# Kernel tuning notes

Measured on AMD Instinct MI355X. Metric: run time of the kernel, lower is better.

The kernel has to match this reference:

```python
import jax, jax.numpy as jnp
import numpy as np

VOCAB, H, B, L = 32000, 1024, 64, 256  # L leaves per complete binary tree


def setup_inputs() -> dict:
    key = jax.random.key(0)
    ks = jax.random.split(key, 12)
    s = 1.0 / np.sqrt(H)
    return {
        "tokens": jax.random.randint(ks[0], (B, L), 0, VOCAB),
        "emb":    jax.random.normal(ks[1], (VOCAB, H), jnp.float32) * 0.02,
        "W_iock": jax.random.normal(ks[2], (H, 3 * H), jnp.float32) * s,
        "b_iock": jax.random.normal(ks[3], (3 * H,), jnp.float32) * s,
        "U_iock": jax.random.normal(ks[4], (H, 3 * H), jnp.float32) * s,
        "W_fl":   jax.random.normal(ks[5], (H, H), jnp.float32) * s,
        "b_fl":   jax.random.normal(ks[6], (H,), jnp.float32) * s,
        "U_fl":   jax.random.normal(ks[7], (H, H), jnp.float32) * s,
        "W_fr":   jax.random.normal(ks[8], (H, H), jnp.float32) * s,
        "b_fr":   jax.random.normal(ks[9], (H,), jnp.float32) * s,
        "U_fr":   jax.random.normal(ks[10], (H, H), jnp.float32) * s,
    }


def _tree_lstm_levels(h, c, W_iock, b_iock, U_iock, W_fl, b_fl, U_fl, W_fr, b_fr, U_fr):
    """Bottom-up level sweep over a complete binary tree.

    h, c: (B, n, H) states of the current level. Each pass merges sibling
    pairs with the BinaryTreeLSTMCell.calculate gate math.
    """
    outs = []
    while h.shape[1] > 1:
        hl, hr = h[:, 0::2], h[:, 1::2]          # (B, n/2, H)
        cl, cr = c[:, 0::2], c[:, 1::2]
        # iock = W_iock(h_left) + U_iock(h_right); split -> i, o, c~
        iock = hl @ W_iock + hr @ U_iock + b_iock
        i_g, o_g, ck = jnp.split(iock, 3, axis=-1)
        fl = jax.nn.sigmoid(hl @ W_fl + hr @ U_fl + b_fl)
        fr = jax.nn.sigmoid(hl @ W_fr + hr @ U_fr + b_fr)
        c = jax.nn.sigmoid(i_g) * jnp.tanh(ck) + fl * cl + fr * cr
        h = jax.nn.sigmoid(o_g) * jnp.tanh(c)
        outs.append(h)
    forest_output = jnp.concatenate(outs, axis=1)  # (B, L-1, H) internal-node hiddens
    return forest_output, h, c


def reference(tokens, emb, W_iock, b_iock, U_iock, W_fl, b_fl, U_fl, W_fr, b_fr, U_fr):
    h = emb[tokens]                 # leaf hidden = embedding, (B, L, H)
    c = jnp.zeros_like(h)           # leaf memory cell = zeros
    forest_output, h_root, c_root = _tree_lstm_levels(
        h, c, W_iock, b_iock, U_iock, W_fl, b_fl, U_fl, W_fr, b_fr, U_fr)
    # (forest_output, (h, c)) with h, c as (1, B, H) like transpose(0, 1)
    return forest_output, (h_root.transpose(1, 0, 2), c_root.transpose(1, 0, 2))
```

## Files before the change

kernel.cpp:

```cpp
#include <hip/hip_runtime.h>
#include <stdint.h>

#define H     1024
#define K2    2048
#define NTOT  5120
#define BATCH 64
#define BM 128
#define BN 128
#define BK 64

typedef unsigned short u16;
typedef __attribute__((ext_vector_type(8))) short short8;
typedef __attribute__((ext_vector_type(4))) float floatx4;

__device__ __forceinline__ float bf2f(u16 u) {
    return __uint_as_float(((uint32_t)u) << 16);
}
__device__ __forceinline__ u16 f2bf(float f) {
    uint32_t u = __float_as_uint(f);
    u += 0x7fffu + ((u >> 16) & 1u);
    return (u16)(u >> 16);
}
__device__ __forceinline__ uint32_t pk2(float lo, float hi) {
    return (uint32_t)f2bf(lo) | ((uint32_t)f2bf(hi) << 16);
}
__device__ __forceinline__ float sigf(float x) {
    return 1.0f / (1.0f + __expf(-x));
}
__device__ __forceinline__ float tanh_(float x) {
    float e = __expf(-2.0f * fabsf(x));
    float r = (1.0f - e) / (1.0f + e);
    return copysignf(r, x);
}

__global__ void fuse_pre(const float* __restrict__ Wio, const float* __restrict__ Uio,
                         const float* __restrict__ Wfl, const float* __restrict__ Ufl,
                         const float* __restrict__ Wfr, const float* __restrict__ Ufr,
                         u16* __restrict__ WT,
                         const int* __restrict__ tokens, const float* __restrict__ emb,
                         u16* __restrict__ leaf) {
    __shared__ u16 tile[32][33];
    int blk = blockIdx.x;
    int t = threadIdx.x;
    if (blk < 10240) {
        int k0 = (blk & 63) * 32;
        int n0 = (blk >> 6) * 32;
        const float *Wp, *Up; int ncols, nloc;
        if (n0 < 3072)      { Wp = Wio; Up = Uio; ncols = 3072; nloc = n0; }
        else if (n0 < 4096) { Wp = Wfl; Up = Ufl; ncols = 1024; nloc = n0 - 3072; }
        else                { Wp = Wfr; Up = Ufr; ncols = 1024; nloc = n0 - 4096; }
        int c = t & 31, r = t >> 5;
#pragma unroll
        for (int i = 0; i < 4; ++i) {
            int rr = r + i * 8;
            int k = k0 + rr;
            float v = (k < 1024) ? Wp[(long)k * ncols + nloc + c]
                                 : Up[(long)(k - 1024) * ncols + nloc + c];
            tile[rr][c] = f2bf(v);
        }
        __syncthreads();
#pragma unroll
        for (int i = 0; i < 4; ++i) {
            int rr = r + i * 8;
            WT[(long)(n0 + rr) * K2 + k0 + c] = tile[c][rr];
        }
    } else {
        int idx = (blk - 10240) * 256 + t;
        int node = idx >> 8;
        int d4 = idx & 255;
        int tok = tokens[node];
        float4 v = ((const float4*)emb)[(long)tok * 256 + d4];
        uint2 o; o.x = pk2(v.x, v.y); o.y = pk2(v.z, v.w);
        ((uint2*)leaf)[(long)node * 256 + d4] = o;
    }
}

__global__ void gemm_bt(const u16* __restrict__ A, const u16* __restrict__ BT,
                        float* __restrict__ G, int mc) {
    __shared__ __align__(16) u16 AsBs[16896];
    u16* As = AsBs;
    u16* Bs = AsBs + 8192;
    float* epi = (float*)AsBs;
    int tid  = threadIdx.x;
    int lane = tid & 63;
    int w    = tid >> 6;
    int wm   = w >> 1, wn = w & 1;
    int rowTile = blockIdx.x * BM;
    int n0      = blockIdx.y * BN;

    const u16* asrc[4];
    const u16* bsrc[4];
#pragma unroll
    for (int cc = 0; cc < 4; ++cc) {
        int r = cc * 32 + w * 8 + (lane >> 3);
        int j = rowTile + r; if (j >= mc) j = mc - 1;
        asrc[cc] = A + (long)j * K2 + (lane & 7) * 8;
        bsrc[cc] = BT + (long)(n0 + r) * K2 + (lane & 7) * 8;
    }

    floatx4 acc[4][4];
#pragma unroll
    for (int mt = 0; mt < 4; ++mt)
#pragma unroll
        for (int nt = 0; nt < 4; ++nt)
            acc[mt][nt] = (floatx4){0.f, 0.f, 0.f, 0.f};

    for (int k0 = 0; k0 < K2; k0 += BK) {
#pragma unroll
        for (int cc = 0; cc < 4; ++cc) {
            __builtin_amdgcn_global_load_lds(
                (const __attribute__((address_space(1))) void*)(asrc[cc] + k0),
                (__attribute__((address_space(3))) void*)(As + cc * 2048 + w * 512), 16, 0, 0);
            __builtin_amdgcn_global_load_lds(
                (const __attribute__((address_space(1))) void*)(bsrc[cc] + k0),
                (__attribute__((address_space(3))) void*)(Bs + cc * 2048 + w * 512), 16, 0, 0);
        }
        __syncthreads();
#pragma unroll
        for (int kb = 0; kb < 2; ++kb) {
            int kfo = kb * 32 + (lane >> 4) * 8;
            short8 af[4], bfv[4];
#pragma unroll
            for (int mt = 0; mt < 4; ++mt)
                af[mt] = *(const short8*)&As[(wm * 64 + mt * 16 + (lane & 15)) * BK + kfo];
#pragma unroll
            for (int nt = 0; nt < 4; ++nt)
                bfv[nt] = *(const short8*)&Bs[(wn * 64 + nt * 16 + (lane & 15)) * BK + kfo];
#pragma unroll
            for (int mt = 0; mt < 4; ++mt)
#pragma unroll
                for (int nt = 0; nt < 4; ++nt)
                    acc[mt][nt] = __builtin_amdgcn_mfma_f32_16x16x32_bf16(
                        af[mt], bfv[nt], acc[mt][nt], 0, 0, 0);
        }
        __syncthreads();
    }

#pragma unroll
    for (int s = 0; s < 2; ++s) {
        if (wm == s) {
#pragma unroll
            for (int mt = 0; mt < 4; ++mt)
#pragma unroll
                for (int r = 0; r < 4; ++r) {
                    int lrow = mt * 16 + (lane >> 4) * 4 + r;
#pragma unroll
                    for (int nt = 0; nt < 4; ++nt)
                        epi[lrow * 132 + wn * 64 + nt * 16 + (lane & 15)] = acc[mt][nt][r];
                }
        }
        __syncthreads();
        int gr0 = rowTile + s * 64;
#pragma unroll
        for (int k = 0; k < 8; ++k) {
            int f4 = tid + k * 256;
            int row = f4 >> 5, c4 = f4 & 31;
            if (gr0 + row < mc) {
                float4 v = *(const float4*)&epi[row * 132 + c4 * 4];
                *(float4*)&G[(long)(gr0 + row) * NTOT + n0 + c4 * 4] = v;
            }
        }
        __syncthreads();
    }
}

#define SWZ2(r) (((r) >> 1) & 3)

#define GP_WAIT(VM)                                                                  \
    asm volatile("s_waitcnt vmcnt(" #VM ") lgkmcnt(0)\n\ts_barrier" ::: "memory")

__global__ __launch_bounds__(512, 4) void gemmP128(const u16* __restrict__ A,
                                                   const u16* __restrict__ BT,
                                                   const float* __restrict__ bio,
                                                   const float* __restrict__ bfl,
                                                   const float* __restrict__ bfr,
                                                   const void* __restrict__ c_in,
                                                   void* __restrict__ c_out, int c_bf16,
                                                   float* __restrict__ outF,
                                                   u16* __restrict__ hnext,
                                                   int lp, int level_off, int gm) {
    __shared__ __align__(16) u16 lds[28672];
    const int tid  = threadIdx.x;
    const int lane = tid & 63;
    const int w    = tid >> 6;
    const int wm   = w >> 1;
    const int wd   = w & 1;

    int f = blockIdx.x;
    int xcd = f & 7, c = f >> 3;
    int by = (xcd & 1) * 8 + (c & 7);
    int bx = (xcd >> 1) * (gm >> 2) + (c >> 3);
    long rowTile = (long)bx * 128;
    int d0 = by * 64;

    const u16* srcA[2];
    {
        int rr_ = w * 16 + (lane >> 2);
        int ck_ = ((lane & 3) ^ SWZ2(rr_)) * 8;
#pragma unroll
        for (int cc = 0; cc < 2; ++cc)
            srcA[cc] = A + (rowTile + rr_) * (long)K2 + cc * 32 + ck_;
    }
    const u16* srcB[5];
    {
        int sr_ = (w >> 1) * 16 + (lane >> 2);
        int ck_ = ((lane & 3) ^ SWZ2(sr_)) * 8;
#pragma unroll
        for (int g = 0; g < 5; ++g)
            srcB[g] = BT + (long)(g * 1024 + d0 + sr_) * K2 + (w & 1) * 32 + ck_;
    }

    const int qv = lane >> 4;
    int rA[2];
#pragma unroll
    for (int mf = 0; mf < 2; ++mf) {
        int rg = wm * 32 + mf * 16 + (lane & 15);
        rA[mf] = rg * 32 + ((qv ^ SWZ2(rg)) * 8);
    }
    int rB[2];
#pragma unroll
    for (int sub = 0; sub < 2; ++sub) {
        int rb = wd * 32 + sub * 16 + (lane & 15);
        rB[sub] = rb * 32 + ((qv ^ SWZ2(rb)) * 8);
    }

    floatx4 acc[2][10];
#pragma unroll
    for (int mf = 0; mf < 2; ++mf)
#pragma unroll
        for (int nf = 0; nf < 10; ++nf)
            acc[mf][nf] = (floatx4){0.f, 0.f, 0.f, 0.f};

#define GP_STG_A(TT)                                                                 \
    do {                                                                             \
        _Pragma("unroll")                                                            \
        for (int cc = 0; cc < 2; ++cc)                                               \
            __builtin_amdgcn_global_load_lds(                                        \
                (const __attribute__((address_space(1))) void*)(srcA[cc] + (TT) * 64),\
                (__attribute__((address_space(3))) void*)(lds + cc * 4096 + tid * 8), 16, 0, 0); \
    } while (0)

#define GP_STG_B(TT, GG)                                                             \
    __builtin_amdgcn_global_load_lds(                                                \
        (const __attribute__((address_space(1))) void*)(srcB[GG] + (TT) * 64),       \
        (__attribute__((address_space(3))) void*)(lds + 8192 + (GG) * 4096 + (w & 1) * 2048 + (w >> 1) * 512 + lane * 8), 16, 0, 0)

#define GP_MFMA(GG)                                                                  \
    do {                                                                             \
        __builtin_amdgcn_s_setprio(1);                                               \
        _Pragma("unroll")                                                            \
        for (int ks = 0; ks < 2; ++ks)                                               \
            _Pragma("unroll")                                                        \
            for (int mf = 0; mf < 2; ++mf)                                           \
                _Pragma("unroll")                                                    \
                for (int sub = 0; sub < 2; ++sub)                                    \
                    acc[mf][(GG) * 2 + sub] = __builtin_amdgcn_mfma_f32_16x16x32_bf16( \
                        aF[ks][mf], bF[ks][sub], acc[mf][(GG) * 2 + sub], 0, 0, 0);  \
        __builtin_amdgcn_s_setprio(0);                                               \
    } while (0)

#define GP_READ_A_B0()                                                               \
    do {                                                                             \
        _Pragma("unroll")                                                            \
        for (int ks = 0; ks < 2; ++ks) {                                             \
            _Pragma("unroll")                                                        \
            for (int mf = 0; mf < 2; ++mf)                                           \
                aF[ks][mf] = *(const short8*)&lds[rA[mf] + ks * 4096];               \
            _Pragma("unroll")                                                        \
            for (int sub = 0; sub < 2; ++sub)                                        \
                bF[ks][sub] = *(const short8*)&lds[8192 + ks * 2048 + rB[sub]];      \
        }                                                                            \
    } while (0)

#define GP_READ_B(GG)                                                                \
    do {                                                                             \
        _Pragma("unroll")                                                            \
        for (int ks = 0; ks < 2; ++ks)                                               \
            _Pragma("unroll")                                                        \
            for (int sub = 0; sub < 2; ++sub)                                        \
                bF[ks][sub] = *(const short8*)&lds[8192 + (GG) * 4096 + ks * 2048 + rB[sub]]; \
    } while (0)

    GP_STG_A(0);
    GP_STG_B(0, 0); GP_STG_B(0, 1); GP_STG_B(0, 2); GP_STG_B(0, 3);

    short8 aF[2][2], bF[2][2];
    for (int t = 0; t < 31; ++t) {
        GP_WAIT(3);
        GP_READ_A_B0();
        GP_STG_B(t, 4);
        GP_MFMA(0);
        GP_WAIT(3);
        GP_READ_B(1);
        GP_STG_A(t + 1);
        GP_MFMA(1);
        GP_WAIT(4);
        GP_READ_B(2);
        GP_STG_B(t + 1, 0);
        GP_MFMA(2);
        GP_WAIT(4);
        GP_READ_B(3);
        GP_STG_B(t + 1, 1);
        GP_MFMA(3);
        GP_WAIT(4);
        GP_READ_B(4);
        GP_STG_B(t + 1, 2);
        GP_STG_B(t + 1, 3);
        GP_MFMA(4);
    }
    GP_WAIT(3);
    GP_READ_A_B0();
    GP_STG_B(31, 4);
    GP_MFMA(0);
    GP_WAIT(3);
    GP_READ_B(1);
    GP_MFMA(1);
    GP_WAIT(2);
    GP_READ_B(2);
    GP_MFMA(2);
    GP_WAIT(1);
    GP_READ_B(3);
    GP_MFMA(3);
    GP_WAIT(0);
    GP_READ_B(4);
    GP_MFMA(4);

#undef GP_STG_A
#undef GP_STG_B
#undef GP_MFMA
#undef GP_READ_A_B0
#undef GP_READ_B

    float bI[2], bO[2], bC[2], bL[2], bR[2];
    int dsub[2];
#pragma unroll
    for (int sub = 0; sub < 2; ++sub) {
        int dd = d0 + wd * 32 + sub * 16 + (lane & 15);
        dsub[sub] = dd;
        bI[sub] = bio[dd]; bO[sub] = bio[1024 + dd]; bC[sub] = bio[2048 + dd];
        bL[sub] = bfl[dd]; bR[sub] = bfr[dd];
    }
    int pmask = (1 << lp) - 1;
    int has_c = (c_in != nullptr);
#pragma unroll
    for (int mf = 0; mf < 2; ++mf) {
#pragma unroll
        for (int rr = 0; rr < 4; ++rr) {
            int row = wm * 32 + mf * 16 + (lane >> 4) * 4 + rr;
            long J = rowTile + row;
            int b = (int)(J >> lp), p = (int)(J & pmask);
            long ho = ((long)b * 255 + level_off + p) * H;
#pragma unroll
            for (int sub = 0; sub < 2; ++sub) {
                int dd = dsub[sub];
                float i_  = acc[mf][0 + sub][rr] + bI[sub];
                float o_  = acc[mf][2 + sub][rr] + bO[sub];
                float ck_ = acc[mf][4 + sub][rr] + bC[sub];
                float cv = sigf(i_) * tanh_(ck_);
                if (has_c) {
                    float fl_ = sigf(acc[mf][6 + sub][rr] + bL[sub]);
                    float fr_ = sigf(acc[mf][8 + sub][rr] + bR[sub]);
                    float cl, cr;
                    if (c_bf16) {
                        cl = bf2f(__builtin_nontemporal_load(
                                 (const u16*)c_in + (2 * J) * H + dd));
                        cr = bf2f(__builtin_nontemporal_load(
                                 (const u16*)c_in + (2 * J + 1) * H + dd));
                    } else {
                        cl = __builtin_nontemporal_load(
                                 (const float*)c_in + (2 * J) * H + dd);
                        cr = __builtin_nontemporal_load(
                                 (const float*)c_in + (2 * J + 1) * H + dd);
                    }
                    cv += fl_ * cl + fr_ * cr;
                }
                float hv = sigf(o_) * tanh_(cv);
                __builtin_nontemporal_store(hv, &outF[ho + dd]);
                if (c_bf16)
                    __builtin_nontemporal_store(f2bf(cv), (u16*)c_out + J * H + dd);
                else
                    __builtin_nontemporal_store(cv, (float*)c_out + J * H + dd);
                __builtin_nontemporal_store(f2bf(hv), hnext + J * H + dd);
            }
        }
    }
}

__global__ __launch_bounds__(512, 4) void gemmS(const u16* __restrict__ A,
                                                const u16* __restrict__ BT,
                                                float* __restrict__ P,
                                                int RT, int KS, int NT,
                                                int mLim, int mPad) {
    __shared__ __align__(16) u16 lds[28672];
    const int tid  = threadIdx.x;
    const int lane = tid & 63;
    const int w    = tid >> 6;
    const int wm   = w >> 1;
    const int wd   = w & 1;

    int nwg = RT * 16 * KS;
    int f = blockIdx.x;
    int q = nwg >> 3, r = nwg & 7;
    int xcd = f & 7, rank = f >> 3;
    int wg = (xcd < r ? xcd * (q + 1) : r * (q + 1) + (xcd - r) * q) + rank;
    int bx  = wg % RT;
    int by  = (wg / RT) % 16;
    int ksx = wg / (RT * 16);
    long rowTile = (long)bx * 128;
    int d0 = by * 64;
    int kOff = ksx * (NT * 64);

    const u16* srcA[2];
    {
        int rr_ = w * 16 + (lane >> 2);
        int ck_ = ((lane & 3) ^ SWZ2(rr_)) * 8;
#pragma unroll
        for (int cc = 0; cc < 2; ++cc)
            srcA[cc] = A + (rowTile + rr_) * (long)K2 + kOff + cc * 32 + ck_;
    }
    const u16* srcB[5];
    {
        int sr_ = (w >> 1) * 16 + (lane >> 2);
        int ck_ = ((lane & 3) ^ SWZ2(sr_)) * 8;
#pragma unroll
        for (int g = 0; g < 5; ++g)
            srcB[g] = BT + (long)(g * 1024 + d0 + sr_) * K2 + kOff + (w & 1) * 32 + ck_;
    }

    const int qv = lane >> 4;
    int rA[2];
#pragma unroll
    for (int mf = 0; mf < 2; ++mf) {
        int rg = wm * 32 + mf * 16 + (lane & 15);
        rA[mf] = rg * 32 + ((qv ^ SWZ2(rg)) * 8);
    }
    int rB[2];
#pragma unroll
    for (int sub = 0; sub < 2; ++sub) {
        int rb = wd * 32 + sub * 16 + (lane & 15);
        rB[sub] = rb * 32 + ((qv ^ SWZ2(rb)) * 8);
    }

    floatx4 acc[2][10];
#pragma unroll
    for (int mf = 0; mf < 2; ++mf)
#pragma unroll
        for (int nf = 0; nf < 10; ++nf)
            acc[mf][nf] = (floatx4){0.f, 0.f, 0.f, 0.f};

#define GS_STG_A(TT)                                                                 \
    do {                                                                             \
        _Pragma("unroll")                                                            \
        for (int cc = 0; cc < 2; ++cc)                                               \
            __builtin_amdgcn_global_load_lds(                                        \
                (const __attribute__((address_space(1))) void*)(srcA[cc] + (TT) * 64),\
                (__attribute__((address_space(3))) void*)(lds + cc * 4096 + tid * 8), 16, 0, 0); \
    } while (0)

#define GS_STG_B(TT, GG)                                                             \
    __builtin_amdgcn_global_load_lds(                                                \
        (const __attribute__((address_space(1))) void*)(srcB[GG] + (TT) * 64),       \
        (__attribute__((address_space(3))) void*)(lds + 8192 + (GG) * 4096 + (w & 1) * 2048 + (w >> 1) * 512 + lane * 8), 16, 0, 0)

#define GS_MFMA(GG)                                                                  \
    do {                                                                             \
        __builtin_amdgcn_s_setprio(1);                                               \
        _Pragma("unroll")                                                            \
        for (int ks = 0; ks < 2; ++ks)                                               \
            _Pragma("unroll")                                                        \
            for (int mf = 0; mf < 2; ++mf)                                           \
                _Pragma("unroll")                                                    \
                for (int sub = 0; sub < 2; ++sub)                                    \
                    acc[mf][(GG) * 2 + sub] = __builtin_amdgcn_mfma_f32_16x16x32_bf16( \
                        aF[ks][mf], bF[ks][sub], acc[mf][(GG) * 2 + sub], 0, 0, 0);  \
        __builtin_amdgcn_s_setprio(0);                                               \
    } while (0)

#define GS_READ_A_B0()                                                               \
    do {                                                                             \
        _Pragma("unroll")                                                            \
        for (int ks = 0; ks < 2; ++ks) {                                             \
            _Pragma("unroll")                                                        \
            for (int mf = 0; mf < 2; ++mf)                                           \
                aF[ks][mf] = *(const short8*)&lds[rA[mf] + ks * 4096];               \
            _Pragma("unroll")                                                        \
            for (int sub = 0; sub < 2; ++sub)                                        \
                bF[ks][sub] = *(const short8*)&lds[8192 + ks * 2048 + rB[sub]];      \
        }                                                                            \
    } while (0)

#define GS_READ_B(GG)                                                                \
    do {                                                                             \
        _Pragma("unroll")                                                            \
        for (int ks = 0; ks < 2; ++ks)                                               \
            _Pragma("unroll")                                                        \
            for (int sub = 0; sub < 2; ++sub)                                        \
                bF[ks][sub] = *(const short8*)&lds[8192 + (GG) * 4096 + ks * 2048 + rB[sub]]; \
    } while (0)

    GS_STG_A(0);
    GS_STG_B(0, 0); GS_STG_B(0, 1); GS_STG_B(0, 2); GS_STG_B(0, 3);

    short8 aF[2][2], bF[2][2];
    for (int t = 0; t < NT - 1; ++t) {
        GP_WAIT(3);
        GS_READ_A_B0();
        GS_STG_B(t, 4);
        GS_MFMA(0);
        GP_WAIT(3);
        GS_READ_B(1);
        GS_STG_A(t + 1);
        GS_MFMA(1);
        GP_WAIT(4);
        GS_READ_B(2);
        GS_STG_B(t + 1, 0);
        GS_MFMA(2);
        GP_WAIT(4);
        GS_READ_B(3);
        GS_STG_B(t + 1, 1);
        GS_MFMA(3);
        GP_WAIT(4);
        GS_READ_B(4);
        GS_STG_B(t + 1, 2);
        GS_STG_B(t + 1, 3);
        GS_MFMA(4);
    }
    GP_WAIT(3);
    GS_READ_A_B0();
    GS_STG_B(NT - 1, 4);
    GS_MFMA(0);
    GP_WAIT(3);
    GS_READ_B(1);
    GS_MFMA(1);
    GP_WAIT(2);
    GS_READ_B(2);
    GS_MFMA(2);
    GP_WAIT(1);
    GS_READ_B(3);
    GS_MFMA(3);
    GP_WAIT(0);
    GS_READ_B(4);
    GS_MFMA(4);

#undef GS_STG_A
#undef GS_STG_B
#undef GS_MFMA
#undef GS_READ_A_B0
#undef GS_READ_B

    int dsub[2];
#pragma unroll
    for (int sub = 0; sub < 2; ++sub)
        dsub[sub] = d0 + wd * 32 + sub * 16 + (lane & 15);
#pragma unroll
    for (int mf = 0; mf < 2; ++mf) {
#pragma unroll
        for (int rr = 0; rr < 4; ++rr) {
            int row = wm * 32 + mf * 16 + (lane >> 4) * 4 + rr;
            long J = rowTile + row;
            if (J < mLim) {
                long pb = ((long)ksx * mPad + J) * NTOT;
#pragma unroll
                for (int g = 0; g < 5; ++g)
#pragma unroll
                    for (int sub = 0; sub < 2; ++sub)
                        P[pb + g * 1024 + dsub[sub]] = acc[mf][g * 2 + sub][rr];
            }
        }
    }
}

__global__ void redgate(const float* __restrict__ P, const float* __restrict__ bio,
                        const float* __restrict__ bfl, const float* __restrict__ bfr,
                        const void* __restrict__ c_in, void* __restrict__ c_out, int c_bf16,
                        float* __restrict__ outF, u16* __restrict__ hnext,
                        int lp, int level_off, int mc, int KS, int mPad) {
    int idx = blockIdx.x * 256 + threadIdx.x;
    int j = idx >> 8;
    if (j >= mc) return;
    int d = (idx & 255) * 4;
    int b = j >> lp, p = j & ((1 << lp) - 1);
    float ac[5][4] = {};
    for (int s = 0; s < KS; ++s) {
        long pb = ((long)s * mPad + j) * NTOT + d;
#pragma unroll
        for (int g = 0; g < 5; ++g) {
            float4 v = *(const float4*)&P[pb + g * 1024];
            ac[g][0] += v.x; ac[g][1] += v.y; ac[g][2] += v.z; ac[g][3] += v.w;
        }
    }
    float4 bi = *(const float4*)&bio[d];
    float4 bo = *(const float4*)&bio[1024 + d];
    float4 bc = *(const float4*)&bio[2048 + d];
    float4 bl = *(const float4*)&bfl[d];
    float4 br = *(const float4*)&bfr[d];
    const float* fbi = (const float*)&bi; const float* fbo = (const float*)&bo;
    const float* fbc = (const float*)&bc; const float* fbl = (const float*)&bl;
    const float* fbr = (const float*)&br;
    float clv[4], crv[4];
    {
        long cb = ((long)b * (2 << lp) + 2 * p) * H + d;
        if (c_bf16) {
            uint2 ul = *(const uint2*)((const u16*)c_in + cb);
            uint2 ur = *(const uint2*)((const u16*)c_in + cb + H);
            clv[0] = bf2f((u16)ul.x); clv[1] = bf2f((u16)(ul.x >> 16));
            clv[2] = bf2f((u16)ul.y); clv[3] = bf2f((u16)(ul.y >> 16));
            crv[0] = bf2f((u16)ur.x); crv[1] = bf2f((u16)(ur.x >> 16));
            crv[2] = bf2f((u16)ur.y); crv[3] = bf2f((u16)(ur.y >> 16));
        } else {
            float4 l4 = *(const float4*)((const float*)c_in + cb);
            float4 r4 = *(const float4*)((const float*)c_in + cb + H);
            clv[0] = l4.x; clv[1] = l4.y; clv[2] = l4.z; clv[3] = l4.w;
            crv[0] = r4.x; crv[1] = r4.y; crv[2] = r4.z; crv[3] = r4.w;
        }
    }
    float cv[4], hv[4];
#pragma unroll
    for (int qq = 0; qq < 4; ++qq) {
        float c = sigf(ac[0][qq] + fbi[qq]) * tanh_(ac[2][qq] + fbc[qq]);
        c += sigf(ac[3][qq] + fbl[qq]) * clv[qq] + sigf(ac[4][qq] + fbr[qq]) * crv[qq];
        cv[qq] = c;
        hv[qq] = sigf(ac[1][qq] + fbo[qq]) * tanh_(c);
    }
    long co = (long)j * H + d;
    if (c_bf16) {
        uint2 oc; oc.x = pk2(cv[0], cv[1]); oc.y = pk2(cv[2], cv[3]);
        *(uint2*)((u16*)c_out + co) = oc;
    } else {
        *(float4*)((float*)c_out + co) = make_float4(cv[0], cv[1], cv[2], cv[3]);
    }
    long oi = ((long)b * 255 + level_off + p) * H + d;
    *(float4*)&outF[oi] = make_float4(hv[0], hv[1], hv[2], hv[3]);
    uint2 oh; oh.x = pk2(hv[0], hv[1]); oh.y = pk2(hv[2], hv[3]);
    *(uint2*)(hnext + (long)j * H + d) = oh;
}

__global__ void gates(const float* __restrict__ G, const float* __restrict__ bio,
                      const float* __restrict__ bfl, const float* __restrict__ bfr,
                      const void* __restrict__ c_in, void* __restrict__ c_out, int c_bf16,
                      float* __restrict__ outF, u16* __restrict__ hnext,
                      int lp, int level_off, int row0, int mc) {
    int idx = blockIdx.x * 256 + threadIdx.x;
    int j = idx >> 8;
    if (j >= mc) return;
    int d = (idx & 255) * 4;
    int J = row0 + j;
    int b = J >> lp, p = J & ((1 << lp) - 1);
    long gb = (long)j * NTOT;
    float4 gi = *(const float4*)&G[gb + d];
    float4 go = *(const float4*)&G[gb + 1024 + d];
    float4 gc = *(const float4*)&G[gb + 2048 + d];
    float4 gl = *(const float4*)&G[gb + 3072 + d];
    float4 gr = *(const float4*)&G[gb + 4096 + d];
    float4 bi = *(const float4*)&bio[d];
    float4 bo = *(const float4*)&bio[1024 + d];
    float4 bc = *(const float4*)&bio[2048 + d];
    float4 bl = *(const float4*)&bfl[d];
    float4 br = *(const float4*)&bfr[d];
    float clv[4] = {0.f, 0.f, 0.f, 0.f}, crv[4] = {0.f, 0.f, 0.f, 0.f};
    if (c_in) {
        long cb = ((long)b * (2 << lp) + 2 * p) * H + d;
        if (c_bf16) {
            uint2 ul = *(const uint2*)((const u16*)c_in + cb);
            uint2 ur = *(const uint2*)((const u16*)c_in + cb + H);
            clv[0] = bf2f((u16)ul.x); clv[1] = bf2f((u16)(ul.x >> 16));
            clv[2] = bf2f((u16)ul.y); clv[3] = bf2f((u16)(ul.y >> 16));
            crv[0] = bf2f((u16)ur.x); crv[1] = bf2f((u16)(ur.x >> 16));
            crv[2] = bf2f((u16)ur.y); crv[3] = bf2f((u16)(ur.y >> 16));
        } else {
            float4 l4 = *(const float4*)((const float*)c_in + cb);
            float4 r4 = *(const float4*)((const float*)c_in + cb + H);
            clv[0] = l4.x; clv[1] = l4.y; clv[2] = l4.z; clv[3] = l4.w;
            crv[0] = r4.x; crv[1] = r4.y; crv[2] = r4.z; crv[3] = r4.w;
        }
    }
    const float* fgi = (const float*)&gi; const float* fgo = (const float*)&go;
    const float* fgc = (const float*)&gc; const float* fgl = (const float*)&gl;
    const float* fgr = (const float*)&gr;
    const float* fbi = (const float*)&bi; const float* fbo = (const float*)&bo;
    const float* fbc = (const float*)&bc; const float* fbl = (const float*)&bl;
    const float* fbr = (const float*)&br;
    float cv[4], hv[4];
    int has_c = (c_in != nullptr);
#pragma unroll
    for (int qq = 0; qq < 4; ++qq) {
        float c = sigf(fgi[qq] + fbi[qq]) * tanh_(fgc[qq] + fbc[qq]);
        if (has_c)
            c += sigf(fgl[qq] + fbl[qq]) * clv[qq] + sigf(fgr[qq] + fbr[qq]) * crv[qq];
        cv[qq] = c;
        hv[qq] = sigf(fgo[qq] + fbo[qq]) * tanh_(c);
    }
    long co = (long)J * H + d;
    if (c_bf16) {
        uint2 oc; oc.x = pk2(cv[0], cv[1]); oc.y = pk2(cv[2], cv[3]);
        *(uint2*)((u16*)c_out + co) = oc;
    } else {
        *(float4*)((float*)c_out + co) = make_float4(cv[0], cv[1], cv[2], cv[3]);
    }
    long oi = ((long)b * 255 + level_off + p) * H + d;
    *(float4*)&outF[oi] = make_float4(hv[0], hv[1], hv[2], hv[3]);
    uint2 oh; oh.x = pk2(hv[0], hv[1]); oh.y = pk2(hv[2], hv[3]);
    *(uint2*)(hnext + (long)J * H + d) = oh;
}

__global__ void root_copy(const float* __restrict__ outF, const void* __restrict__ c_root,
                          int c_bf16, float* __restrict__ tail) {
    int idx = blockIdx.x * 256 + threadIdx.x;
    if (idx < 65536) {
        int b = idx >> 10, d = idx & 1023;
        tail[idx] = outF[((long)b * 255 + 254) * H + d];
    } else {
        int i2 = idx - 65536;
        tail[idx] = c_bf16 ? bf2f(((const u16*)c_root)[i2]) : ((const float*)c_root)[i2];
    }
}

extern "C" void kernel_launch(void* const* d_in, const int* in_sizes, int n_in,
                              void* d_out, int out_size, void* d_ws, size_t ws_size,
                              hipStream_t stream) {
    const int* tokens = (const int*)d_in[0];
    const float* emb = (const float*)d_in[1];
    const float* Wio = (const float*)d_in[2];
    const float* bio = (const float*)d_in[3];
    const float* Uio = (const float*)d_in[4];
    const float* Wfl = (const float*)d_in[5];
    const float* bfl = (const float*)d_in[6];
    const float* Ufl = (const float*)d_in[7];
    const float* Wfr = (const float*)d_in[8];
    const float* bfr = (const float*)d_in[9];
    const float* Ufr = (const float*)d_in[10];
    float* outF = (float*)d_out;

    char* ws = (char*)d_ws;
    size_t off = 0;
    u16* WT   = (u16*)(ws + off); off += (size_t)NTOT * K2 * 2;
    u16* leaf = (u16*)(ws + off); off += (size_t)BATCH * 256 * H * 2;
    u16* hE   = (u16*)(ws + off); off += (size_t)8192 * H * 2;
    u16* hO   = (u16*)(ws + off); off += (size_t)4096 * H * 2;
    size_t cEf = (size_t)8192 * H, cOf = (size_t)4096 * H;
    int c_bf16 = (ws_size >= off + (cEf + cOf) * 4 + (size_t)512 * NTOT * 4) ? 0 : 1;
    size_t csz = c_bf16 ? 2 : 4;
    void* cE = (void*)(ws + off); off += cEf * csz;
    void* cO = (void*)(ws + off); off += cOf * csz;
    size_t avail = (ws_size > off) ? (ws_size - off) : 0;
    size_t Pbytes = (size_t)2048 * NTOT * 4;
    int splitOK = (avail >= Pbytes);
    float* P = (float*)(ws + off);
    long Grows = (long)(avail / ((size_t)NTOT * 4));
    if (Grows > 512) Grows = 512;
    Grows &= ~127L;
    if (Grows < 128) Grows = 128;
    float* G = (float*)(ws + off);

    fuse_pre<<<26624, 256, 0, stream>>>(Wio, Uio, Wfl, Ufl, Wfr, Ufr, WT,
                                        tokens, emb, leaf);

    const int off_out[8] = {0, 128, 192, 224, 240, 248, 252, 254};
    for (int li = 0; li < 8; ++li) {
        int lp = 7 - li;
        long m = (long)BATCH << lp;
        const u16* Acur = (li == 0) ? leaf : ((li & 1) ? hE : hO);
        u16* hnext = (li & 1) ? hO : hE;
        const void* c_in = (li == 0) ? nullptr : ((li & 1) ? cE : cO);
        void* c_out = (li & 1) ? cO : cE;
        if (m >= 2048) {
            int gm = (int)(m >> 7);
            gemmP128<<<gm * 16, 512, 0, stream>>>(Acur, WT, bio, bfl, bfr,
                                                  c_in, c_out, c_bf16, outF, hnext,
                                                  lp, off_out[li], gm);
        } else if (splitOK) {
            int KS = (m == 1024) ? 2 : (m == 512) ? 4 : (m == 256) ? 8 : 16;
            int RT = (m >= 128) ? (int)(m >> 7) : 1;
            int mPad = RT * 128;
            int NT = 32 / KS;
            gemmS<<<RT * 16 * KS, 512, 0, stream>>>(Acur, WT, P, RT, KS, NT,
                                                    (int)m, mPad);
            redgate<<<(int)m, 256, 0, stream>>>(P, bio, bfl, bfr, c_in, c_out, c_bf16,
                                                outF, hnext, lp, off_out[li],
                                                (int)m, KS, mPad);
        } else {
            for (long row0 = 0; row0 < m; row0 += Grows) {
                int mc = (int)((m - row0 > Grows) ? Grows : (m - row0));
                dim3 grid((mc + BM - 1) / BM, NTOT / BN);
                gemm_bt<<<grid, 256, 0, stream>>>(Acur + row0 * K2, WT, G, mc);
                gates<<<mc, 256, 0, stream>>>(G, bio, bfl, bfr, c_in, c_out, c_bf16,
                                              outF, hnext, lp, off_out[li], (int)row0, mc);
            }
        }
    }
    root_copy<<<512, 256, 0, stream>>>(outF, cO, c_bf16, outF + (size_t)BATCH * 255 * H);
}
```

Measured before the change: 666.6 us.

## Fuse small tree levels into one persistent kernel with grid barriers

Replaces the per-level split-K GEMM plus reduce/gate launches for the five smallest levels (and the root copy) with a single persistent 256-block kernel. Inside it, levels are separated by software grid-wide barriers built on atomic counters. This removes roughly eleven kernel launches and their launch gaps on the latency-bound tail of the tree. The cost is spin-wait barrier overhead, a fixed 256-block tiling, and a reliance on all blocks being co-resident to avoid deadlock.

```diff
diff --git a/kernel.cpp b/kernel.cpp
--- a/kernel.cpp
+++ b/kernel.cpp
@@ -386,23 +386,30 @@
     }
 }
 
-__global__ __launch_bounds__(512, 4) void gemmS(const u16* __restrict__ A,
-                                                const u16* __restrict__ BT,
-                                                float* __restrict__ P,
-                                                int RT, int KS, int NT,
-                                                int mLim, int mPad) {
-    __shared__ __align__(16) u16 lds[28672];
-    const int tid  = threadIdx.x;
+__device__ __forceinline__ void gsync(int* bar, int target) {
+    __threadfence();
+    __syncthreads();
+    if (threadIdx.x == 0) {
+        atomicAdd(bar, 1);
+        while (atomicAdd(bar, 0) < target)
+            __builtin_amdgcn_s_sleep(2);
+    }
+    __syncthreads();
+    __threadfence();
+}
+
+__device__ __forceinline__ void gemmS_body(const u16* __restrict__ A,
+                                           const u16* __restrict__ BT,
+                                           float* __restrict__ P,
+                                           int RT, int KS, int NT, int mLim, int mPad,
+                                           u16* lds, int blk, int tid) {
     const int lane = tid & 63;
-    const int w    = tid >> 6;
-    const int wm   = w >> 1;
-    const int wd   = w & 1;
-
-    int nwg = RT * 16 * KS;
-    int f = blockIdx.x;
-    int q = nwg >> 3, r = nwg & 7;
-    int xcd = f & 7, rank = f >> 3;
-    int wg = (xcd < r ? xcd * (q + 1) : r * (q + 1) + (xcd - r) * q) + rank;
+    const int w = tid >> 6;
+    const int wm = w >> 1;
+    const int wd = w & 1;
+
+    int xcd = blk & 7, rank = blk >> 3;
+    int wg = xcd * 32 + rank;
     int bx  = wg % RT;
     int by  = (wg / RT) % 16;
     int ksx = wg / (RT * 16);
@@ -570,14 +577,16 @@
     }
 }
 
-__global__ void redgate(const float* __restrict__ P, const float* __restrict__ bio,
-                        const float* __restrict__ bfl, const float* __restrict__ bfr,
-                        const void* __restrict__ c_in, void* __restrict__ c_out, int c_bf16,
-                        float* __restrict__ outF, u16* __restrict__ hnext,
-                        int lp, int level_off, int mc, int KS, int mPad) {
-    int idx = blockIdx.x * 256 + threadIdx.x;
+__device__ __forceinline__ void redgate_item(int idx, const float* __restrict__ P,
+                                             const float* __restrict__ bio,
+                                             const float* __restrict__ bfl,
+                                             const float* __restrict__ bfr,
+                                             const void* __restrict__ c_in,
+                                             void* __restrict__ c_out, int c_bf16,
+                                             float* __restrict__ outF,
+                                             u16* __restrict__ hnext,
+                                             int lp, int level_off, int KS, int mPad) {
     int j = idx >> 8;
-    if (j >= mc) return;
     int d = (idx & 255) * 4;
     int b = j >> lp, p = j & ((1 << lp) - 1);
     float ac[5][4] = {};
@@ -633,6 +642,53 @@
     *(float4*)&outF[oi] = make_float4(hv[0], hv[1], hv[2], hv[3]);
     uint2 oh; oh.x = pk2(hv[0], hv[1]); oh.y = pk2(hv[2], hv[3]);
     *(uint2*)(hnext + (long)j * H + d) = oh;
+}
+
+__global__ __launch_bounds__(512, 4) void small_levels(const u16* __restrict__ BT,
+                                                       u16* hE, u16* hO,
+                                                       void* cE, void* cO, int c_bf16,
+                                                       const float* __restrict__ bio,
+                                                       const float* __restrict__ bfl,
+                                                       const float* __restrict__ bfr,
+                                                       float* __restrict__ outF,
+                                                       float* __restrict__ P,
+                                                       int* bar) {
+    __shared__ __align__(16) u16 lds[28672];
+    const int tid = threadIdx.x;
+    const int blk = blockIdx.x;
+    int sn = 0;
+#pragma unroll 1
+    for (int li = 3; li < 8; ++li) {
+        int lp = 7 - li;
+        int m = BATCH << lp;
+        const u16* A = (li & 1) ? hE : hO;
+        u16* hnext   = (li & 1) ? hO : hE;
+        const void* c_in = (li & 1) ? cE : cO;
+        void* c_out      = (li & 1) ? cO : cE;
+        int level_off = 256 - (2 << lp);
+        int KS = (m == 1024) ? 2 : (m == 512) ? 4 : (m == 256) ? 8 : 16;
+        int RT = (m >= 128) ? (m >> 7) : 1;
+        int NT = 32 / KS;
+        int mPad = RT * 128;
+        gemmS_body(A, BT, P, RT, KS, NT, m, mPad, lds, blk, tid);
+        gsync(bar, 256 * ++sn);
+        int items = m * 256;
+        for (int idx = blk * 512 + tid; idx < items; idx += 256 * 512)
+            redgate_item(idx, P, bio, bfl, bfr, c_in, c_out, c_bf16,
+                         outF, hnext, lp, level_off, KS, mPad);
+        gsync(bar, 256 * ++sn);
+    }
+    {
+        int idx = blk * 512 + tid;
+        float* tail = outF + (size_t)BATCH * 255 * H;
+        if (idx < 65536) {
+            int b = idx >> 10, d = idx & 1023;
+            tail[idx] = outF[((long)b * 255 + 254) * H + d];
+        } else {
+            int i2 = idx - 65536;
+            tail[idx] = c_bf16 ? bf2f(((const u16*)cO)[i2]) : ((const float*)cO)[i2];
+        }
+    }
 }
 
 __global__ void gates(const float* __restrict__ G, const float* __restrict__ bio,
@@ -744,41 +800,46 @@
     void* cO = (void*)(ws + off); off += cOf * csz;
     size_t avail = (ws_size > off) ? (ws_size - off) : 0;
     size_t Pbytes = (size_t)2048 * NTOT * 4;
-    int splitOK = (avail >= Pbytes);
+    int splitOK = (avail >= Pbytes + 1024);
     float* P = (float*)(ws + off);
+    int* bar = (int*)(ws + off + Pbytes);
     long Grows = (long)(avail / ((size_t)NTOT * 4));
     if (Grows > 512) Grows = 512;
     Grows &= ~127L;
     if (Grows < 128) Grows = 128;
     float* G = (float*)(ws + off);
 
+    if (splitOK)
+        hipMemsetAsync(bar, 0, 64, stream);
+
     fuse_pre<<<26624, 256, 0, stream>>>(Wio, Uio, Wfl, Ufl, Wfr, Ufr, WT,
                                         tokens, emb, leaf);
 
     const int off_out[8] = {0, 128, 192, 224, 240, 248, 252, 254};
-    for (int li = 0; li < 8; ++li) {
+    for (int li = 0; li < 3; ++li) {
         int lp = 7 - li;
         long m = (long)BATCH << lp;
         const u16* Acur = (li == 0) ? leaf : ((li & 1) ? hE : hO);
         u16* hnext = (li & 1) ? hO : hE;
         const void* c_in = (li == 0) ? nullptr : ((li & 1) ? cE : cO);
         void* c_out = (li & 1) ? cO : cE;
-        if (m >= 2048) {
-            int gm = (int)(m >> 7);
-            gemmP128<<<gm * 16, 512, 0, stream>>>(Acur, WT, bio, bfl, bfr,
-                                                  c_in, c_out, c_bf16, outF, hnext,
-                                                  lp, off_out[li], gm);
-        } else if (splitOK) {
-            int KS = (m == 1024) ? 2 : (m == 512) ? 4 : (m == 256) ? 8 : 16;
-            int RT = (m >= 128) ? (int)(m >> 7) : 1;
-            int mPad = RT * 128;
-            int NT = 32 / KS;
-            gemmS<<<RT * 16 * KS, 512, 0, stream>>>(Acur, WT, P, RT, KS, NT,
-                                                    (int)m, mPad);
-            redgate<<<(int)m, 256, 0, stream>>>(P, bio, bfl, bfr, c_in, c_out, c_bf16,
-                                                outF, hnext, lp, off_out[li],
-                                                (int)m, KS, mPad);
-        } else {
+        int gm = (int)(m >> 7);
+        gemmP128<<<gm * 16, 512, 0, stream>>>(Acur, WT, bio, bfl, bfr,
+                                              c_in, c_out, c_bf16, outF, hnext,
+                                              lp, off_out[li], gm);
+    }
+
+    if (splitOK) {
+        small_levels<<<256, 512, 0, stream>>>(WT, hE, hO, cE, cO, c_bf16,
+                                              bio, bfl, bfr, outF, P, bar);
+    } else {
+        for (int li = 3; li < 8; ++li) {
+            int lp = 7 - li;
+            long m = (long)BATCH << lp;
+            const u16* Acur = (li & 1) ? hE : hO;
+            u16* hnext = (li & 1) ? hO : hE;
+            const void* c_in = (li & 1) ? cE : cO;
+            void* c_out = (li & 1) ? cO : cE;
             for (long row0 = 0; row0 < m; row0 += Grows) {
                 int mc = (int)((m - row0 > Grows) ? Grows : (m - row0));
                 dim3 grid((mc + BM - 1) / BM, NTOT / BN);
@@ -787,6 +848,6 @@
                                               outF, hnext, lp, off_out[li], (int)row0, mc);
             }
         }
-    }
-    root_copy<<<512, 256, 0, stream>>>(outF, cO, c_bf16, outF + (size_t)BATCH * 255 * H);
-}
+        root_copy<<<512, 256, 0, stream>>>(outF, cO, c_bf16, outF + (size_t)BATCH * 255 * H);
+    }
+}
```

Result: slower. 1.667 ms (+150.0%).
